# Optimization experiments

Measured on AMD Instinct MI355X. Metric: run time of the kernel, lower is better.

The kernel has to match this reference:

```python
import jax, jax.numpy as jnp
import numpy as np

N_HEAD = 10

def setup_inputs() -> dict:
    key = jax.random.key(0)
    k1, k2, k3 = jax.random.split(key, 3)
    n_embd = 640
    x = jax.random.normal(k1, (4, 2048, n_embd), dtype=jnp.float32)
    w_qkv = jax.random.normal(k2, (3 * n_embd, n_embd), dtype=jnp.float32) * (1.0 / np.sqrt(n_embd))
    w_proj = jax.random.normal(k3, (n_embd, n_embd), dtype=jnp.float32) * (1.0 / np.sqrt(n_embd))
    return {"x": x, "w_qkv": w_qkv, "w_proj": w_proj}

def reference(x, w_qkv, w_proj):
    bsz, seqlen, n_embd = x.shape
    head_dim = n_embd // N_HEAD
    qkv = jnp.einsum('bsd,ed->bse', x, w_qkv)  # [B,S,3E]
    q, k, v = jnp.split(qkv, 3, axis=2)
    # [B,H,S,Dh]
    q = q.reshape(bsz, seqlen, N_HEAD, head_dim).transpose(0, 2, 1, 3)
    k = k.reshape(bsz, seqlen, N_HEAD, head_dim).transpose(0, 2, 1, 3)
    v = v.reshape(bsz, seqlen, N_HEAD, head_dim).transpose(0, 2, 1, 3)
    scale = 1.0 / np.sqrt(head_dim).astype(np.float32)
    scores = jnp.einsum('bhqd,bhkd->bhqk', q, k) * scale
    causal = jnp.tril(jnp.ones((seqlen, seqlen), dtype=bool))
    scores = jnp.where(causal, scores, jnp.finfo(scores.dtype).min)
    attn = jax.nn.softmax(scores, axis=-1)
    y = jnp.einsum('bhqk,bhkd->bhqd', attn, v)
    y = y.transpose(0, 2, 1, 3).reshape(bsz, seqlen, n_embd)
    return jnp.einsum('bsd,ed->bse', y, w_proj)
```

## Files before the change

### kernel.cpp

```cpp
#include <hip/hip_runtime.h>

#define BB 4
#define SS 2048
#define EE 640
#define NHH 10
#define DHH 64
#define MTOK 8192
#define E33 1920

#if __has_builtin(__builtin_amdgcn_exp2f)
#define EXP2(x) __builtin_amdgcn_exp2f(x)
#else
#define EXP2(x) exp2f(x)
#endif

#define QSCALE 0.18033688011112042f

typedef float f32x4 __attribute__((ext_vector_type(4)));
typedef __bf16 bf16x8 __attribute__((ext_vector_type(8)));
typedef __bf16 bf16x4 __attribute__((ext_vector_type(4)));
typedef unsigned short u16;
typedef u16 u16x4 __attribute__((ext_vector_type(4)));

__device__ inline u16 bfbits(float f) {
  return __builtin_bit_cast(u16, (__bf16)f);
}

__device__ __forceinline__ void gl_lds16(const u16* g, u16* l) {
  __builtin_amdgcn_global_load_lds(
      (const __attribute__((address_space(1))) unsigned int*)g,
      (__attribute__((address_space(3))) unsigned int*)l, 16, 0, 0);
}

#define XN4   1310720
#define WQN4   307200
#define WPN4   102400
__global__ void convert_all(const float* __restrict__ x, const float* __restrict__ wqkv,
                            const float* __restrict__ wproj,
                            u16* __restrict__ xb, u16* __restrict__ wqkvb,
                            u16* __restrict__ wprojb) {
  int i = blockIdx.x * blockDim.x + threadIdx.x;
  const float* src; u16* dst; int off;
  if (i < XN4)              { src = x;     dst = xb;     off = i; }
  else if (i < XN4 + WQN4)  { src = wqkv;  dst = wqkvb;  off = i - XN4; }
  else if (i < XN4 + WQN4 + WPN4) { src = wproj; dst = wprojb; off = i - XN4 - WQN4; }
  else return;
  float4 v = ((const float4*)src)[off];
  u16x4 o = { bfbits(v.x), bfbits(v.y), bfbits(v.z), bfbits(v.w) };
  ((u16x4*)dst)[off] = o;
}

__global__ __launch_bounds__(256) void gemm_qkv(
    const u16* __restrict__ A, const u16* __restrict__ Bt,
    u16* __restrict__ qb, u16* __restrict__ kb, u16* __restrict__ vt) {
  __shared__ __align__(16) u16 As[2][128 * 64];
  __shared__ __align__(16) u16 Bs[2][128 * 64];
  const int t = threadIdx.x;
  const int orig = blockIdx.x;
  const int newid = (orig & 7) * 120 + (orig >> 3);
  const int m0 = (newid / 15) * 128;
  const int n0 = (newid % 15) * 128;
  const int w = t >> 6, lane = t & 63, n16 = lane & 15, quad = lane >> 4;
  const int wm = w >> 1, wn = w & 1;

  const int sub = lane >> 3, cL = lane & 7;
  const int srcColE = (cL ^ sub) * 8;
  const int rd0 = (quad ^ (n16 & 7)) * 8;
  const int rd1 = ((4 + quad) ^ (n16 & 7)) * 8;

  f32x4 acc[4][4];
  for (int i = 0; i < 4; i++)
    for (int j = 0; j < 4; j++) acc[i][j] = f32x4{0.f, 0.f, 0.f, 0.f};

#pragma unroll
  for (int i = 0; i < 4; ++i) {
    int c = w * 4 + i, row = c * 8 + sub;
    gl_lds16(&A[(m0 + row) * 640 + srcColE], &As[0][c * 512]);
    gl_lds16(&Bt[(n0 + row) * 640 + srcColE], &Bs[0][c * 512]);
  }
  __syncthreads();

  for (int kt = 0; kt < 10; ++kt) {
    const int cur = kt & 1, nxt = cur ^ 1;
    if (kt < 9) {
#pragma unroll
      for (int i = 0; i < 4; ++i) {
        int c = w * 4 + i, row = c * 8 + sub;
        gl_lds16(&A[(m0 + row) * 640 + (kt + 1) * 64 + srcColE], &As[nxt][c * 512]);
        gl_lds16(&Bt[(n0 + row) * 640 + (kt + 1) * 64 + srcColE], &Bs[nxt][c * 512]);
      }
    }
#pragma unroll
    for (int ks = 0; ks < 2; ++ks) {
      const int rd = ks ? rd1 : rd0;
      bf16x8 a[4], b[4];
      for (int mi = 0; mi < 4; mi++)
        a[mi] = *(const bf16x8*)&As[cur][(wm * 64 + mi * 16 + n16) * 64 + rd];
      for (int ni = 0; ni < 4; ni++)
        b[ni] = *(const bf16x8*)&Bs[cur][(wn * 64 + ni * 16 + n16) * 64 + rd];
      for (int mi = 0; mi < 4; mi++)
        for (int ni = 0; ni < 4; ni++)
          acc[mi][ni] = __builtin_amdgcn_mfma_f32_16x16x32_bf16(a[mi], b[ni], acc[mi][ni], 0, 0, 0);
    }
    __syncthreads();
  }

  const int which = n0 / 640;
  for (int ni = 0; ni < 4; ni++) {
    int col = n0 + wn * 64 + ni * 16 + n16;
    int eh = col - which * 640;
    int h = eh >> 6, d = eh & 63;
    for (int mi = 0; mi < 4; mi++) {
      int tb = m0 + wm * 64 + mi * 16 + quad * 4;
      f32x4 c = acc[mi][ni];
      if (which == 0) {
        c[0] *= QSCALE; c[1] *= QSCALE; c[2] *= QSCALE; c[3] *= QSCALE;
      }
      if (which == 2) {
        int b_ = tb >> 11, s_ = tb & 2047;
        u16x4 pk = { bfbits(c[0]), bfbits(c[1]), bfbits(c[2]), bfbits(c[3]) };
        *(u16x4*)&vt[((b_ * NHH + h) * DHH + d) * SS + s_] = pk;
      } else {
        u16* dst = (which == 0) ? qb : kb;
        for (int r = 0; r < 4; r++) {
          int tok = tb + r;
          int b_ = tok >> 11, s_ = tok & 2047;
          dst[((b_ * NHH + h) * SS + s_) * DHH + d] = bfbits(c[r]);
        }
      }
    }
  }
}

__global__ __launch_bounds__(256) void attn_kernel(
    const u16* __restrict__ qb, const u16* __restrict__ kb, const u16* __restrict__ vt,
    u16* __restrict__ y) {
  __shared__ __align__(16) u16 Ks[2][64 * 64];
  __shared__ __align__(16) u16 Vs[2][64 * 64];
  const int t = threadIdx.x;
  const int w = t >> 6, lane = t & 63, n16 = lane & 15, quad = lane >> 4;
  const int bh = blockIdx.x;
  const int qt = 31 - blockIdx.y;
  const int qb0 = qt * 64;
  const int b_ = bh / NHH, h = bh % NHH;

  bf16x8 aq[2];
  {
    const u16* qp = &qb[(bh * SS + qb0 + w * 16 + n16) * DHH];
    aq[0] = *(const bf16x8*)&qp[quad * 8];
    aq[1] = *(const bf16x8*)&qp[32 + quad * 8];
  }
  const int q_rel = w * 16 + n16;

  const int c1 = 256 + t;
  const int row0 = t >> 3,  g0 = t & 7;
  const int row1 = c1 >> 3, g1 = c1 & 7;
  auto perm = [](int k) {
    int p = k >> 5, rem = k & 31, qd = rem >> 3, tt = rem & 7;
    return ((p << 1) | (tt >> 2)) * 16 + qd * 4 + (tt & 3);
  };
  const int prow0 = perm(row0), prow1 = perm(row1);
  const int kw0 = prow0 * 64 + ((g0 ^ (prow0 & 7)) * 8);
  const int kw1 = prow1 * 64 + ((g1 ^ (prow1 & 7)) * 8);
  const int vw0 = row0 * 64 + ((g0 ^ (row0 & 7)) * 8);
  const int vw1 = row1 * 64 + ((g1 ^ (row1 & 7)) * 8);
  const int col0 = g0 * 8, col1 = g1 * 8;
  const int rdA = (quad ^ (n16 & 7)) * 8;
  const int rdB = ((4 + quad) ^ (n16 & 7)) * 8;

  float4 fk0, fk1, fv0, fv1;
  fk0 = *(const float4*)&kb[(bh * SS + row0) * DHH + col0];
  fk1 = *(const float4*)&kb[(bh * SS + row1) * DHH + col1];
  fv0 = *(const float4*)&vt[(bh * DHH + row0) * SS + col0];
  fv1 = *(const float4*)&vt[(bh * DHH + row1) * SS + col1];
  *(float4*)&Ks[0][kw0] = fk0;
  *(float4*)&Ks[0][kw1] = fk1;
  *(float4*)&Vs[0][vw0] = fv0;
  *(float4*)&Vs[0][vw1] = fv1;

  float m_i = -1e30f, l_i = 0.f;
  f32x4 o[4];
  for (int db = 0; db < 4; db++) o[db] = f32x4{0.f, 0.f, 0.f, 0.f};

  for (int kt = 0; kt <= qt; ++kt) {
    __syncthreads();
    const int cur = kt & 1, nxt = cur ^ 1;
    if (kt < qt) {
      int kk = (kt + 1) * 64;
      fk0 = *(const float4*)&kb[(bh * SS + kk + row0) * DHH + col0];
      fk1 = *(const float4*)&kb[(bh * SS + kk + row1) * DHH + col1];
      fv0 = *(const float4*)&vt[(bh * DHH + row0) * SS + kk + col0];
      fv1 = *(const float4*)&vt[(bh * DHH + row1) * SS + kk + col1];
    }

    f32x4 sc[4];
#pragma unroll
    for (int nb = 0; nb < 4; nb++) {
      f32x4 c = f32x4{0.f, 0.f, 0.f, 0.f};
      bf16x8 ak0 = *(const bf16x8*)&Ks[cur][(nb * 16 + n16) * 64 + rdA];
      c = __builtin_amdgcn_mfma_f32_16x16x32_bf16(ak0, aq[0], c, 0, 0, 0);
      bf16x8 ak1 = *(const bf16x8*)&Ks[cur][(nb * 16 + n16) * 64 + rdB];
      c = __builtin_amdgcn_mfma_f32_16x16x32_bf16(ak1, aq[1], c, 0, 0, 0);
      sc[nb] = c;
    }

    if (kt == qt) {
#pragma unroll
      for (int nb = 0; nb < 4; nb++)
#pragma unroll
        for (int r = 0; r < 4; r++) {
          int key = ((nb >> 1) << 5) + quad * 8 + ((nb & 1) << 2) + r;
          if (key > q_rel) sc[nb][r] = -1e30f;
        }
    }

    f32x4 mx;
#pragma unroll
    for (int r = 0; r < 4; r++)
      mx[r] = fmaxf(fmaxf(sc[0][r], sc[1][r]), fmaxf(sc[2][r], sc[3][r]));
    float rm = fmaxf(fmaxf(mx[0], mx[1]), fmaxf(mx[2], mx[3]));
    rm = fmaxf(rm, __shfl_xor(rm, 16));
    rm = fmaxf(rm, __shfl_xor(rm, 32));

    if (!__all(rm - m_i <= 8.0f)) {
      float mnew = fmaxf(m_i, rm);
      float alpha = EXP2(m_i - mnew);
      l_i *= alpha;
#pragma unroll
      for (int db = 0; db < 4; db++)
#pragma unroll
        for (int r = 0; r < 4; r++) o[db][r] *= alpha;
      m_i = mnew;
    }

    f32x4 ps[4];
#pragma unroll
    for (int nb = 0; nb < 4; nb++)
#pragma unroll
      for (int r = 0; r < 4; r++) ps[nb][r] = EXP2(sc[nb][r] - m_i);
    f32x4 sv;
#pragma unroll
    for (int r = 0; r < 4; r++)
      sv[r] = (ps[0][r] + ps[1][r]) + (ps[2][r] + ps[3][r]);
    float rs = (sv[0] + sv[1]) + (sv[2] + sv[3]);
    rs += __shfl_xor(rs, 16);
    rs += __shfl_xor(rs, 32);
    l_i += rs;

#pragma unroll
    for (int p2 = 0; p2 < 2; p2++) {
      bf16x8 bp;
#pragma unroll
      for (int j = 0; j < 4; j++) {
        bp[j]     = (__bf16)ps[2 * p2][j];
        bp[4 + j] = (__bf16)ps[2 * p2 + 1][j];
      }
      const int rdV = p2 ? rdB : rdA;
#pragma unroll
      for (int db = 0; db < 4; db++) {
        bf16x8 av = *(const bf16x8*)&Vs[cur][(db * 16 + n16) * 64 + rdV];
        o[db] = __builtin_amdgcn_mfma_f32_16x16x32_bf16(av, bp, o[db], 0, 0, 0);
      }
    }

    if (kt < qt) {
      *(float4*)&Ks[nxt][kw0] = fk0;
      *(float4*)&Ks[nxt][kw1] = fk1;
      *(float4*)&Vs[nxt][vw0] = fv0;
      *(float4*)&Vs[nxt][vw1] = fv1;
    }
  }

  const float inv = 1.0f / l_i;
  const int tok = b_ * SS + qb0 + w * 16 + n16;
#pragma unroll
  for (int db = 0; db < 4; db++) {
    bf16x4 pk = { (__bf16)(o[db][0] * inv), (__bf16)(o[db][1] * inv),
                  (__bf16)(o[db][2] * inv), (__bf16)(o[db][3] * inv) };
    *(bf16x4*)&y[tok * EE + h * DHH + db * 16 + quad * 4] = pk;
  }
}

__global__ __launch_bounds__(256) void gemm_proj(
    const u16* __restrict__ A, const u16* __restrict__ Bt, float* __restrict__ out) {
  __shared__ __align__(16) u16 As[2][128 * 64];
  __shared__ __align__(16) u16 Bs[2][128 * 64];
  const int t = threadIdx.x;
  const int orig = blockIdx.x;
  const int newid = (orig & 7) * 40 + (orig >> 3);
  const int m0 = (newid / 5) * 128;
  const int n0 = (newid % 5) * 128;
  const int w = t >> 6, lane = t & 63, n16 = lane & 15, quad = lane >> 4;
  const int wm = w >> 1, wn = w & 1;

  const int sub = lane >> 3, cL = lane & 7;
  const int srcColE = (cL ^ sub) * 8;
  const int rd0 = (quad ^ (n16 & 7)) * 8;
  const int rd1 = ((4 + quad) ^ (n16 & 7)) * 8;

  f32x4 acc[4][4];
  for (int i = 0; i < 4; i++)
    for (int j = 0; j < 4; j++) acc[i][j] = f32x4{0.f, 0.f, 0.f, 0.f};

#pragma unroll
  for (int i = 0; i < 4; ++i) {
    int c = w * 4 + i, row = c * 8 + sub;
    gl_lds16(&A[(m0 + row) * 640 + srcColE], &As[0][c * 512]);
    gl_lds16(&Bt[(n0 + row) * 640 + srcColE], &Bs[0][c * 512]);
  }
  __syncthreads();

  for (int kt = 0; kt < 10; ++kt) {
    const int cur = kt & 1, nxt = cur ^ 1;
    if (kt < 9) {
#pragma unroll
      for (int i = 0; i < 4; ++i) {
        int c = w * 4 + i, row = c * 8 + sub;
        gl_lds16(&A[(m0 + row) * 640 + (kt + 1) * 64 + srcColE], &As[nxt][c * 512]);
        gl_lds16(&Bt[(n0 + row) * 640 + (kt + 1) * 64 + srcColE], &Bs[nxt][c * 512]);
      }
    }
#pragma unroll
    for (int ks = 0; ks < 2; ++ks) {
      const int rd = ks ? rd1 : rd0;
      bf16x8 a[4], b[4];
      for (int mi = 0; mi < 4; mi++)
        a[mi] = *(const bf16x8*)&As[cur][(wm * 64 + mi * 16 + n16) * 64 + rd];
      for (int ni = 0; ni < 4; ni++)
        b[ni] = *(const bf16x8*)&Bs[cur][(wn * 64 + ni * 16 + n16) * 64 + rd];
      for (int mi = 0; mi < 4; mi++)
        for (int ni = 0; ni < 4; ni++)
          acc[mi][ni] = __builtin_amdgcn_mfma_f32_16x16x32_bf16(a[mi], b[ni], acc[mi][ni], 0, 0, 0);
    }
    __syncthreads();
  }

  for (int ni = 0; ni < 4; ni++) {
    int col = n0 + wn * 64 + ni * 16 + n16;
    for (int mi = 0; mi < 4; mi++) {
      int rowb = m0 + wm * 64 + mi * 16 + quad * 4;
      f32x4 c = acc[mi][ni];
      for (int r = 0; r < 4; r++) out[(rowb + r) * 640 + col] = c[r];
    }
  }
}

extern "C" void kernel_launch(void* const* d_in, const int* in_sizes, int n_in,
                              void* d_out, int out_size, void* d_ws, size_t ws_size,
                              hipStream_t stream) {
  const float* x     = (const float*)d_in[0];
  const float* wqkv  = (const float*)d_in[1];
  const float* wproj = (const float*)d_in[2];
  float* out = (float*)d_out;

  char* ws = (char*)d_ws;
  u16* xb     = (u16*)(ws + 0);
  u16* wqkvb  = (u16*)(ws + 10485760);
  u16* wprojb = (u16*)(ws + 12943360);
  u16* qbuf   = (u16*)(ws + 13762560);
  u16* kbuf   = (u16*)(ws + 24248320);
  u16* vtb    = (u16*)(ws + 34734080);
  u16* ybuf   = (u16*)(ws + 45219840);

  convert_all<<<6720, 256, 0, stream>>>(x, wqkv, wproj, xb, wqkvb, wprojb);

  gemm_qkv<<<960, 256, 0, stream>>>(xb, wqkvb, qbuf, kbuf, vtb);
  attn_kernel<<<dim3(40, 32), 256, 0, stream>>>(qbuf, kbuf, vtb, ybuf);
  gemm_proj<<<320, 256, 0, stream>>>(ybuf, wprojb, out);
}
```

Before: 169.6 us.

## Fuse fp32-to-bf16 conversion of x into the QKV GEMM tile loads

The QKV GEMM now reads fp32 x directly, converts each tile to bf16 in registers and writes it into the swizzled LDS buffer. The separate conversion pass over x and its bf16 staging copy are removed, and the convert kernel now handles only the weights. In exchange, x is read in fp32 (twice the bytes) by each of the 15 column blocks that share a row tile. The A tile is also staged through registers with extra conversion work instead of the async global-to-LDS path.

```diff
diff --git a/kernel.cpp b/kernel.cpp
--- a/kernel.cpp
+++ b/kernel.cpp
@@ -32,18 +32,14 @@
       (__attribute__((address_space(3))) unsigned int*)l, 16, 0, 0);
 }
 
-#define XN4   1310720
 #define WQN4   307200
 #define WPN4   102400
-__global__ void convert_all(const float* __restrict__ x, const float* __restrict__ wqkv,
-                            const float* __restrict__ wproj,
-                            u16* __restrict__ xb, u16* __restrict__ wqkvb,
-                            u16* __restrict__ wprojb) {
+__global__ void convert_w(const float* __restrict__ wqkv, const float* __restrict__ wproj,
+                          u16* __restrict__ wqkvb, u16* __restrict__ wprojb) {
   int i = blockIdx.x * blockDim.x + threadIdx.x;
   const float* src; u16* dst; int off;
-  if (i < XN4)              { src = x;     dst = xb;     off = i; }
-  else if (i < XN4 + WQN4)  { src = wqkv;  dst = wqkvb;  off = i - XN4; }
-  else if (i < XN4 + WQN4 + WPN4) { src = wproj; dst = wprojb; off = i - XN4 - WQN4; }
+  if (i < WQN4)              { src = wqkv;  dst = wqkvb;  off = i; }
+  else if (i < WQN4 + WPN4)  { src = wproj; dst = wprojb; off = i - WQN4; }
   else return;
   float4 v = ((const float4*)src)[off];
   u16x4 o = { bfbits(v.x), bfbits(v.y), bfbits(v.z), bfbits(v.w) };
@@ -51,7 +47,7 @@
 }
 
 __global__ __launch_bounds__(256) void gemm_qkv(
-    const u16* __restrict__ A, const u16* __restrict__ Bt,
+    const float* __restrict__ X, const u16* __restrict__ Bt,
     u16* __restrict__ qb, u16* __restrict__ kb, u16* __restrict__ vt) {
   __shared__ __align__(16) u16 As[2][128 * 64];
   __shared__ __align__(16) u16 Bs[2][128 * 64];
@@ -68,15 +64,29 @@
   const int rd0 = (quad ^ (n16 & 7)) * 8;
   const int rd1 = ((4 + quad) ^ (n16 & 7)) * 8;
 
+  const int tr = t >> 4;
+  const int tc4 = (t & 15) * 4;
+  const int tg = tc4 >> 3;
+  const int awz = ((tg ^ (tr & 7)) * 8) + (tc4 & 7);
+  const float* xbase = &X[(size_t)(m0 + tr) * 640 + tc4];
+
   f32x4 acc[4][4];
   for (int i = 0; i < 4; i++)
     for (int j = 0; j < 4; j++) acc[i][j] = f32x4{0.f, 0.f, 0.f, 0.f};
 
+  float4 af[8];
+#pragma unroll
+  for (int p = 0; p < 8; ++p)
+    af[p] = *(const float4*)&xbase[p * 16 * 640];
 #pragma unroll
   for (int i = 0; i < 4; ++i) {
     int c = w * 4 + i, row = c * 8 + sub;
-    gl_lds16(&A[(m0 + row) * 640 + srcColE], &As[0][c * 512]);
     gl_lds16(&Bt[(n0 + row) * 640 + srcColE], &Bs[0][c * 512]);
+  }
+#pragma unroll
+  for (int p = 0; p < 8; ++p) {
+    bf16x4 pk = { (__bf16)af[p].x, (__bf16)af[p].y, (__bf16)af[p].z, (__bf16)af[p].w };
+    *(bf16x4*)&As[0][(p * 16 + tr) * 64 + awz] = pk;
   }
   __syncthreads();
 
@@ -86,9 +96,11 @@
 #pragma unroll
       for (int i = 0; i < 4; ++i) {
         int c = w * 4 + i, row = c * 8 + sub;
-        gl_lds16(&A[(m0 + row) * 640 + (kt + 1) * 64 + srcColE], &As[nxt][c * 512]);
         gl_lds16(&Bt[(n0 + row) * 640 + (kt + 1) * 64 + srcColE], &Bs[nxt][c * 512]);
       }
+#pragma unroll
+      for (int p = 0; p < 8; ++p)
+        af[p] = *(const float4*)&xbase[p * 16 * 640 + (kt + 1) * 64];
     }
 #pragma unroll
     for (int ks = 0; ks < 2; ++ks) {
@@ -101,6 +113,13 @@
       for (int mi = 0; mi < 4; mi++)
         for (int ni = 0; ni < 4; ni++)
           acc[mi][ni] = __builtin_amdgcn_mfma_f32_16x16x32_bf16(a[mi], b[ni], acc[mi][ni], 0, 0, 0);
+    }
+    if (kt < 9) {
+#pragma unroll
+      for (int p = 0; p < 8; ++p) {
+        bf16x4 pk = { (__bf16)af[p].x, (__bf16)af[p].y, (__bf16)af[p].z, (__bf16)af[p].w };
+        *(bf16x4*)&As[nxt][(p * 16 + tr) * 64 + awz] = pk;
+      }
     }
     __syncthreads();
   }
@@ -354,7 +373,6 @@
   float* out = (float*)d_out;
 
   char* ws = (char*)d_ws;
-  u16* xb     = (u16*)(ws + 0);
   u16* wqkvb  = (u16*)(ws + 10485760);
   u16* wprojb = (u16*)(ws + 12943360);
   u16* qbuf   = (u16*)(ws + 13762560);
@@ -362,9 +380,9 @@
   u16* vtb    = (u16*)(ws + 34734080);
   u16* ybuf   = (u16*)(ws + 45219840);
 
-  convert_all<<<6720, 256, 0, stream>>>(x, wqkv, wproj, xb, wqkvb, wprojb);
-
-  gemm_qkv<<<960, 256, 0, stream>>>(xb, wqkvb, qbuf, kbuf, vtb);
+  convert_w<<<1600, 256, 0, stream>>>(wqkv, wproj, wqkvb, wprojb);
+
+  gemm_qkv<<<960, 256, 0, stream>>>(x, wqkvb, qbuf, kbuf, vtb);
   attn_kernel<<<dim3(40, 32), 256, 0, stream>>>(qbuf, kbuf, vtb, ybuf);
   gemm_proj<<<320, 256, 0, stream>>>(ybuf, wprojb, out);
 }
```

Result: slower. 181.9 us (+7.2%).
